# Optimization experiments

Measured on AMD Instinct MI355X. Metric: run time of the kernel, lower is better.

Reference implementation:

```python
import jax, jax.numpy as jnp
import numpy as np

DT = 0.001  # integration time step (forward arg dt in the original module)


def force_fn(x):
    # Harmonic well stand-in for the user-supplied force function.
    return -x


def _nh_step(x, v, alpha, kT, mass, Q):
    """One Nose-Hoover step, exactly mirroring the recompute block in backward()."""
    ndof = x.shape[-1]
    v2 = (v * v).sum(-1)
    alpha = alpha + (DT / 4) * (v2 - ndof * kT) / Q
    v = v * jnp.exp(-alpha[..., None] * (DT / 2))
    v2 = (v * v).sum(-1)
    alpha = alpha + (DT / 4) * (v2 - ndof * kT) / Q
    v = v + (DT / 2) * force_fn(x) / mass
    x = x + DT * v
    v = v + (DT / 2) * force_fn(x) / mass
    v2 = (v * v).sum(-1)
    alpha = alpha + (DT / 4) * (v2 - ndof * kT) / Q
    v = v * jnp.exp(-alpha[..., None] * (DT / 2))
    v2 = (v * v).sum(-1)
    alpha = alpha + (DT / 4) * (v2 - ndof * kT) / Q
    return x, v, alpha


def setup_inputs() -> dict:
    key = jax.random.key(0)
    k1, k2 = jax.random.split(key)
    B, D = 4096, 64  # batch of systems, degrees of freedom per system
    return {
        "x0": jax.random.normal(k1, (B, D), jnp.float32),
        "v0": jax.random.normal(k2, (B, D), jnp.float32),
        "alpha0": jnp.zeros((B,), jnp.float32),
        "kT": jnp.ones((), jnp.float32),
        "mass": jnp.ones((), jnp.float32),
        "Q": jnp.ones((), jnp.float32),
        "n_steps": 1000,
        "store_every": 10,
    }


def reference(x0, v0, alpha0, kT, mass, Q, n_steps, store_every):
    n_chunks = n_steps // store_every  # assume divisibility (1000 / 10)

    def inner(c, _):
        x, v, a = c
        return _nh_step(x, v, a, kT, mass, Q), None

    def chunk(c, _):
        c, _ = jax.lax.scan(inner, c, None, length=store_every)
        return c, (c[0], c[1])  # snapshot (x, v) every store_every steps

    _, (xs, vs) = jax.lax.scan(chunk, (x0, v0, alpha0), None, length=n_chunks)
    traj_x = jnp.concatenate([x0[None], xs], axis=0)  # [n_steps//store_every + 1, B, D]
    traj_v = jnp.concatenate([v0[None], vs], axis=0)
    return traj_x, traj_v
```

## Files before the change

### kernel.cpp

```cpp
#include <hip/hip_runtime.h>

#define DT 0.001f

typedef float f4 __attribute__((ext_vector_type(4)));

template<int CTRL>
__device__ __forceinline__ float dpp_add(float v) {
    int r = __builtin_amdgcn_update_dpp(0, __float_as_int(v), CTRL, 0xf, 0xf, false);
    return v + __int_as_float(r);
}

__device__ __forceinline__ float reduce16(float t) {
    t = dpp_add<0x121>(t);
    t = dpp_add<0x122>(t);
    t = dpp_add<0x124>(t);
    t = dpp_add<0x128>(t);
    return t;
}

__device__ __forceinline__ float expm(float z) {
    float p = __builtin_fmaf(z, -0.16666667f, 0.5f);
    p = __builtin_fmaf(z, p, -1.0f);
    p = __builtin_fmaf(z, p, 1.0f);
    return p;
}

__device__ __forceinline__ float sumsq(const f4& v) {
    float ta = v.x * v.x, tb = v.y * v.y, tc = v.z * v.z, td = v.w * v.w;
    return (ta + tb) + (tc + td);
}

template<int SE>
__device__ __forceinline__ void run(f4& x, f4& v, float& alpha, float& r,
                                    int n_chunks, int se_rt,
                                    float c, float cE, float c2E, float hd, float hdt,
                                    f4* outx, f4* outv, int snap4, int fidx)
{
    const int se = (SE > 0) ? SE : se_rt;
    const float c2 = 2.0f * c;
    for (int ck = 1; ck <= n_chunks; ++ck) {
        alpha = __builtin_fmaf(c, r, alpha - cE);
        float s1 = expm(hdt * alpha);
        v *= s1;
        r *= s1 * s1;
        alpha = __builtin_fmaf(c, r, alpha - cE);
        #pragma unroll
        for (int i = 0; i < se - 1; ++i) {
            v -= hd * x;
            x += DT * v;
            v -= hd * x;
            r = reduce16(sumsq(v));
            alpha = __builtin_fmaf(c, r, alpha - cE);
            float s2 = expm(hdt * alpha);
            r *= s2 * s2;
            alpha = __builtin_fmaf(c2, r, alpha - c2E);
            float s1n = expm(hdt * alpha);
            v *= s2 * s1n;
            r *= s1n * s1n;
            alpha = __builtin_fmaf(c, r, alpha - cE);
        }
        v -= hd * x;
        x += DT * v;
        v -= hd * x;
        r = reduce16(sumsq(v));
        alpha = __builtin_fmaf(c, r, alpha - cE);
        float s2 = expm(hdt * alpha);
        v *= s2;
        r *= s2 * s2;
        alpha = __builtin_fmaf(c, r, alpha - cE);
        __builtin_nontemporal_store(x, &outx[(size_t)ck * snap4 + fidx]);
        __builtin_nontemporal_store(v, &outv[(size_t)ck * snap4 + fidx]);
    }
}

__global__ __launch_bounds__(256) void nh_kernel(
    const float* __restrict__ x0, const float* __restrict__ v0,
    const float* __restrict__ alpha0,
    const float* __restrict__ kT_p, const float* __restrict__ mass_p,
    const float* __restrict__ Q_p,
    const int* __restrict__ n_steps_p, const int* __restrict__ store_every_p,
    float* __restrict__ out, int B)
{
    const int D = 64;
    const int gid = blockIdx.x * blockDim.x + threadIdx.x;
    const int sys = gid >> 4;
    const int g   = gid & 15;
    if (sys >= B) return;

    const int n_steps = *n_steps_p;
    const int se      = *store_every_p;
    const int n_chunks = n_steps / se;

    const float kt = *kT_p, m = *mass_p, q = *Q_p;
    const float c   = 0.25f * DT / q;
    const float E   = (float)D * kt;
    const float cE  = c * E;
    const float c2E = 2.0f * cE;
    const float hd  = 0.5f * DT / m;
    const float hdt = 0.5f * DT;

    const int snap4 = B * 16;
    const int fidx  = sys * 16 + g;

    f4 x = ((const f4*)x0)[fidx];
    f4 v = ((const f4*)v0)[fidx];
    float alpha = alpha0[sys];

    f4* outx = (f4*)out;
    f4* outv = ((f4*)out) + (size_t)(n_chunks + 1) * snap4;

    __builtin_nontemporal_store(x, &outx[fidx]);
    __builtin_nontemporal_store(v, &outv[fidx]);

    float r = reduce16(sumsq(v));

    if (se == 10)
        run<10>(x, v, alpha, r, n_chunks, se, c, cE, c2E, hd, hdt, outx, outv, snap4, fidx);
    else
        run<0>(x, v, alpha, r, n_chunks, se, c, cE, c2E, hd, hdt, outx, outv, snap4, fidx);
}

extern "C" void kernel_launch(void* const* d_in, const int* in_sizes, int n_in,
                              void* d_out, int out_size, void* d_ws, size_t ws_size,
                              hipStream_t stream) {
    const float* x0     = (const float*)d_in[0];
    const float* v0     = (const float*)d_in[1];
    const float* alpha0 = (const float*)d_in[2];
    const float* kT     = (const float*)d_in[3];
    const float* mass   = (const float*)d_in[4];
    const float* Q      = (const float*)d_in[5];
    const int* n_steps  = (const int*)d_in[6];
    const int* store_ev = (const int*)d_in[7];

    const int B = in_sizes[0] / 64;
    const int threads = B * 16;
    const int block = 256;
    const int grid = (threads + block - 1) / block;

    nh_kernel<<<grid, block, 0, stream>>>(x0, v0, alpha0, kT, mass, Q,
                                          n_steps, store_ev, (float*)d_out, B);
}
```

Baseline: 272.4 us.

## Spread each system over 32 lanes with float2 and readlane cross-row reduction

Each 64-dof system now maps to 32 threads holding two elements each instead of 16 threads holding four, doubling total thread count. The squared-velocity reduction adds readlane steps after the DPP row reduction to combine two 16-lane rows per system. The aim is more parallelism and shorter per-thread dependency chains in a latency-bound serial integration. In exchange it adds readlane (SGPR round-trip) overhead per step and uses narrower stores.

```diff
diff --git a/kernel.cpp b/kernel.cpp
--- a/kernel.cpp
+++ b/kernel.cpp
@@ -2,7 +2,7 @@
 
 #define DT 0.001f
 
-typedef float f4 __attribute__((ext_vector_type(4)));
+typedef float f2 __attribute__((ext_vector_type(2)));
 
 template<int CTRL>
 __device__ __forceinline__ float dpp_add(float v) {
@@ -10,12 +10,18 @@
     return v + __int_as_float(r);
 }
 
-__device__ __forceinline__ float reduce16(float t) {
+__device__ __forceinline__ float reduce32(float t, bool hi) {
     t = dpp_add<0x121>(t);
     t = dpp_add<0x122>(t);
     t = dpp_add<0x124>(t);
     t = dpp_add<0x128>(t);
-    return t;
+    int ti = __float_as_int(t);
+    float a0 = __int_as_float(__builtin_amdgcn_readlane(ti, 0));
+    float a1 = __int_as_float(__builtin_amdgcn_readlane(ti, 16));
+    float b0 = __int_as_float(__builtin_amdgcn_readlane(ti, 32));
+    float b1 = __int_as_float(__builtin_amdgcn_readlane(ti, 48));
+    float rA = a0 + a1, rB = b0 + b1;
+    return hi ? rB : rA;
 }
 
 __device__ __forceinline__ float expm(float z) {
@@ -25,16 +31,15 @@
     return p;
 }
 
-__device__ __forceinline__ float sumsq(const f4& v) {
-    float ta = v.x * v.x, tb = v.y * v.y, tc = v.z * v.z, td = v.w * v.w;
-    return (ta + tb) + (tc + td);
+__device__ __forceinline__ float sumsq2(const f2& v) {
+    return __builtin_fmaf(v.y, v.y, v.x * v.x);
 }
 
 template<int SE>
-__device__ __forceinline__ void run(f4& x, f4& v, float& alpha, float& r,
+__device__ __forceinline__ void run(f2& x, f2& v, float& alpha, float& r, bool hi,
                                     int n_chunks, int se_rt,
                                     float c, float cE, float c2E, float hd, float hdt,
-                                    f4* outx, f4* outv, int snap4, int fidx)
+                                    f2* outx, f2* outv, int snap2, int fidx)
 {
     const int se = (SE > 0) ? SE : se_rt;
     const float c2 = 2.0f * c;
@@ -49,7 +54,7 @@
             v -= hd * x;
             x += DT * v;
             v -= hd * x;
-            r = reduce16(sumsq(v));
+            r = reduce32(sumsq2(v), hi);
             alpha = __builtin_fmaf(c, r, alpha - cE);
             float s2 = expm(hdt * alpha);
             r *= s2 * s2;
@@ -62,14 +67,14 @@
         v -= hd * x;
         x += DT * v;
         v -= hd * x;
-        r = reduce16(sumsq(v));
+        r = reduce32(sumsq2(v), hi);
         alpha = __builtin_fmaf(c, r, alpha - cE);
         float s2 = expm(hdt * alpha);
         v *= s2;
         r *= s2 * s2;
         alpha = __builtin_fmaf(c, r, alpha - cE);
-        __builtin_nontemporal_store(x, &outx[(size_t)ck * snap4 + fidx]);
-        __builtin_nontemporal_store(v, &outv[(size_t)ck * snap4 + fidx]);
+        __builtin_nontemporal_store(x, &outx[(size_t)ck * snap2 + fidx]);
+        __builtin_nontemporal_store(v, &outv[(size_t)ck * snap2 + fidx]);
     }
 }
 
@@ -83,9 +88,9 @@
 {
     const int D = 64;
     const int gid = blockIdx.x * blockDim.x + threadIdx.x;
-    const int sys = gid >> 4;
-    const int g   = gid & 15;
+    const int sys = gid >> 5;
     if (sys >= B) return;
+    const bool hi = (threadIdx.x & 32) != 0;
 
     const int n_steps = *n_steps_p;
     const int se      = *store_every_p;
@@ -99,25 +104,25 @@
     const float hd  = 0.5f * DT / m;
     const float hdt = 0.5f * DT;
 
-    const int snap4 = B * 16;
-    const int fidx  = sys * 16 + g;
+    const int snap2 = B * 32;
+    const int fidx  = gid;
 
-    f4 x = ((const f4*)x0)[fidx];
-    f4 v = ((const f4*)v0)[fidx];
+    f2 x = ((const f2*)x0)[fidx];
+    f2 v = ((const f2*)v0)[fidx];
     float alpha = alpha0[sys];
 
-    f4* outx = (f4*)out;
-    f4* outv = ((f4*)out) + (size_t)(n_chunks + 1) * snap4;
+    f2* outx = (f2*)out;
+    f2* outv = ((f2*)out) + (size_t)(n_chunks + 1) * snap2;
 
     __builtin_nontemporal_store(x, &outx[fidx]);
     __builtin_nontemporal_store(v, &outv[fidx]);
 
-    float r = reduce16(sumsq(v));
+    float r = reduce32(sumsq2(v), hi);
 
     if (se == 10)
-        run<10>(x, v, alpha, r, n_chunks, se, c, cE, c2E, hd, hdt, outx, outv, snap4, fidx);
+        run<10>(x, v, alpha, r, hi, n_chunks, se, c, cE, c2E, hd, hdt, outx, outv, snap2, fidx);
     else
-        run<0>(x, v, alpha, r, n_chunks, se, c, cE, c2E, hd, hdt, outx, outv, snap4, fidx);
+        run<0>(x, v, alpha, r, hi, n_chunks, se, c, cE, c2E, hd, hdt, outx, outv, snap2, fidx);
 }
 
 extern "C" void kernel_launch(void* const* d_in, const int* in_sizes, int n_in,
@@ -133,7 +138,7 @@
     const int* store_ev = (const int*)d_in[7];
 
     const int B = in_sizes[0] / 64;
-    const int threads = B * 16;
+    const int threads = B * 32;
     const int block = 256;
     const int grid = (threads + block - 1) / block;
 
```

New measurement: 323.5 us. +18.8%, slower.
